# Kernel tuning notes

Measured on AMD Instinct MI355X. Metric: run time of the kernel, lower is better.

## Reference

```python
import jax, jax.numpy as jnp
import numpy as np

DT = 0.01
NUM_STEPS = 2
DIM = 8        # latentDim (q:4, p:4)
HID = 128      # hiddenDim
BATCH = 524288


def _hamiltonian(z, W1, b1, W2, b2, W3, b3):
    # MLP H: (batch, 8) -> (batch,) scalar energy, tanh activations
    h = jnp.tanh(z @ W1 + b1)
    h = jnp.tanh(h @ W2 + b2)
    return (h @ W3 + b3)[..., 0]


def _grad_h(z, W1, b1, W2, b2, W3, b3):
    # dH/dz, batched; mirrors torch.autograd.grad(H.sum(), z)
    # torch detaches z before grad (create_graph keeps param graph)
    zc = jax.lax.stop_gradient(z)
    return jax.grad(lambda zz: _hamiltonian(zz, W1, b1, W2, b2, W3, b3).sum())(zc)


def setup_inputs() -> dict:
    key = jax.random.key(0)
    ks = jax.random.split(key, 7)
    z = jax.random.normal(ks[0], (BATCH, DIM), dtype=jnp.float32)
    W1 = jax.random.normal(ks[1], (DIM, HID), dtype=jnp.float32) / np.float32(np.sqrt(DIM))
    b1 = jnp.zeros((HID,), dtype=jnp.float32)
    W2 = jax.random.normal(ks[2], (HID, HID), dtype=jnp.float32) / np.float32(np.sqrt(HID))
    b2 = jnp.zeros((HID,), dtype=jnp.float32)
    W3 = jax.random.normal(ks[3], (HID, 1), dtype=jnp.float32) / np.float32(np.sqrt(HID))
    b3 = jnp.zeros((1,), dtype=jnp.float32)
    return {"z": z, "W1": W1, "b1": b1, "W2": W2, "b2": b2, "W3": W3, "b3": b3}


def reference(z, W1, b1, W2, b2, W3, b3):
    q, p = jnp.split(z, 2, axis=1)
    for _ in range(NUM_STEPS):
        g = _grad_h(jnp.concatenate([q, p], axis=1), W1, b1, W2, b2, W3, b3)
        dHdq, dHdp = jnp.split(g, 2, axis=1)
        p_half = p - 0.5 * DT * dHdq
        q_new = q + DT * dHdp
        g2 = _grad_h(jnp.concatenate([q_new, p_half], axis=1), W1, b1, W2, b2, W3, b3)
        dHdq_new = jnp.split(g2, 2, axis=1)[0]
        p = p_half - 0.5 * DT * dHdq_new
        q = q_new
    return jnp.concatenate([q, p], axis=1)
```

## Files before the change

kernel.cpp:

```cpp
#include <hip/hip_runtime.h>


typedef float f32x4 __attribute__((ext_vector_type(4)));
typedef int   i32x2 __attribute__((ext_vector_type(2)));
typedef int   i32x4 __attribute__((ext_vector_type(4)));
typedef int   i32x8 __attribute__((ext_vector_type(8)));

#define DT 0.01f
#define S1 64.0f
#define S2 16.0f
#define TWO_LOG2E 2.8853900817779268f
#define SCL1 0x7F7F7F7F

#define OFF_W1B 0
#define OFF_W2B 4096
#define OFF_W2T 20480
#define OFF_W1T 36864
#define WTOT    38912

__device__ __forceinline__ unsigned char to_fp8(float x) {
    return (unsigned char)(__builtin_amdgcn_cvt_pk_fp8_f32(x, x, 0, false) & 0xff);
}
__device__ __forceinline__ float fexp2(float x) {
#if __has_builtin(__builtin_amdgcn_exp2f)
    return __builtin_amdgcn_exp2f(x);
#else
    return exp2f(x);
#endif
}
__device__ __forceinline__ float frcp(float x) {
#if __has_builtin(__builtin_amdgcn_rcpf)
    return __builtin_amdgcn_rcpf(x);
#else
    return 1.0f / x;
#endif
}

__device__ __forceinline__ i32x2 tr8(unsigned char* p) {
#if __has_builtin(__builtin_amdgcn_ds_read_tr8_b64)
    return __builtin_amdgcn_ds_read_tr8_b64((__attribute__((address_space(3))) i32x2*)p);
#else
    i32x2 d;
    asm volatile("ds_read_b64_tr_b8 %0, %1\n\ts_waitcnt lgkmcnt(0)"
                 : "=v"(d)
                 : "v"((unsigned)(unsigned long long)(__attribute__((address_space(3))) void*)p)
                 : "memory");
    __builtin_amdgcn_sched_barrier(0);
    return d;
#endif
}

__device__ __forceinline__ i32x8 read_a(unsigned char* abase) {
    i32x2 a0 = tr8(abase);
    i32x2 a1 = tr8(abase + 512);
    i32x2 a2 = tr8(abase + 1024);
    i32x2 a3 = tr8(abase + 1536);
    return (i32x8){a0[0], a0[1], a1[0], a1[1], a2[0], a2[1], a3[0], a3[1]};
}

__device__ __forceinline__ f32x4 mm128(i32x8 a, i32x8 b, f32x4 c) {
#if __has_builtin(__builtin_amdgcn_mfma_scale_f32_16x16x128_f8f6f4)
    return __builtin_amdgcn_mfma_scale_f32_16x16x128_f8f6f4(a, b, c, 0, 0, 0, SCL1, 0, SCL1);
#else
    #pragma unroll
    for (int kt = 0; kt < 4; kt++) {
        long long aa = ((long long)(unsigned)a[2 * kt + 1] << 32) | (unsigned)a[2 * kt];
        long long bb = ((long long)(unsigned)b[2 * kt + 1] << 32) | (unsigned)b[2 * kt];
        c = __builtin_amdgcn_mfma_f32_16x16x32_fp8_fp8(aa, bb, c, 0, 0, 0);
    }
    return c;
#endif
}

__global__ __launch_bounds__(256) void hnn_prep_kernel(
    const float* __restrict__ W1, const float* __restrict__ W2,
    unsigned char* __restrict__ ws)
{
    const int t = threadIdx.x, b = blockIdx.x;
    if (b == 0) {
        for (int i = t; i < 1024; i += 256) ((int*)(ws + OFF_W1B))[i] = 0;
        for (int i = t; i < 512;  i += 256) ((int*)(ws + OFF_W1T))[i] = 0;
        __syncthreads();
        for (int i = t; i < 1024; i += 256) {
            int row = i >> 7, col = i & 127;
            float w = W1[i];
            ws[OFF_W1B + (col >> 4) * 512 + (col & 15) * 8 + row] = to_fp8(w * TWO_LOG2E);
            int c = col >> 5, h = c >> 1, s = (c & 1) * 8 + (col & 7);
            int qd = (col >> 3) & 3;
            ws[OFF_W1T + (h * 64 + qd * 16 + row) * 16 + s] = to_fp8(w);
        }
    } else {
        int idx = (b - 1) * 256 + t;
        int row = idx >> 7, col = idx & 127;
        float w = W2[idx];
        {
            int c = row >> 5, h = c >> 1, s = (c & 1) * 8 + (row & 7);
            int qd = (row >> 3) & 3;
            ws[OFF_W2B + (((col >> 4) * 2 + h) * 64 + qd * 16 + (col & 15)) * 16 + s] =
                to_fp8(w * TWO_LOG2E);
        }
        {
            int c = col >> 5, h = c >> 1, s = (c & 1) * 8 + (col & 7);
            int qd = (col >> 3) & 3;
            ws[OFF_W2T + (((row >> 4) * 2 + h) * 64 + qd * 16 + (row & 15)) * 16 + s] =
                to_fp8(w * 4.0f);
        }
    }
}

__global__ __launch_bounds__(256) void hnn_leapfrog_kernel(
    const float* __restrict__ Z, const unsigned char* __restrict__ WS,
    const float* __restrict__ B1f, const float* __restrict__ B2f,
    const float* __restrict__ W3, float* __restrict__ OUT)
{
    __shared__ __align__(16) unsigned char sWT[WTOT];
    __shared__ __align__(16) unsigned char sACT[4 * 2048];
    __shared__ __align__(16) float sZ[512];

    const int t   = threadIdx.x;
    const int blk = blockIdx.x;

    for (int i = t; i < WTOT / 16; i += 256)
        __builtin_amdgcn_global_load_lds(
            (const __attribute__((address_space(1))) void*)(WS + i * 16),
            (__attribute__((address_space(3))) void*)(sWT + i * 16), 16, 0, 0);
    sZ[t]       = Z[blk * 512 + t];
    sZ[t + 256] = Z[blk * 512 + 256 + t];

    const int lane = t & 63;
    const int wv   = t >> 6;
    const int nn   = lane & 15;
    const int qd   = lane >> 4;

    float b1v[8], b2v[8], w3v[8];
    #pragma unroll
    for (int nt = 0; nt < 8; nt++) {
        b1v[nt] = B1f[nt * 16 + nn] * TWO_LOG2E;
        b2v[nt] = B2f[nt * 16 + nn] * TWO_LOG2E;
        w3v[nt] = W3[nt * 16 + nn] * (4.0f * S2);
    }
    __syncthreads();

    unsigned char* act   = sACT + wv * 2048;
    float*         zrow  = sZ + wv * 128;
    unsigned char* abase = act + qd * 128 + nn;
    unsigned char* awr   = act + nn * 16 + qd * 4;

    #pragma unroll 1
    for (int ev = 0; ev < 4; ev++) {
        long long az = 0;
        if (qd == 0) {
            const f32x4* zr = (const f32x4*)(zrow + nn * 8);
            f32x4 z0 = zr[0], z1 = zr[1];
            int lo = __builtin_amdgcn_cvt_pk_fp8_f32(z0[0], z0[1], 0, false);
            lo     = __builtin_amdgcn_cvt_pk_fp8_f32(z0[2], z0[3], lo, true);
            int hi = __builtin_amdgcn_cvt_pk_fp8_f32(z1[0], z1[1], 0, false);
            hi     = __builtin_amdgcn_cvt_pk_fp8_f32(z1[2], z1[3], hi, true);
            az = ((long long)(unsigned)hi << 32) | (unsigned)lo;
        }
        float hc[8][4];
        #pragma unroll
        for (int nt = 0; nt < 8; nt++) {
            long long bf = *(const long long*)(sWT + OFF_W1B + nt * 512 + lane * 8);
            f32x4 c = {b1v[nt], b1v[nt], b1v[nt], b1v[nt]};
            c = __builtin_amdgcn_mfma_f32_16x16x32_fp8_fp8(az, bf, c, 0, 0, 0);
            #pragma unroll
            for (int r = 0; r < 4; r++) {
                float e  = fexp2(c[r]);
                float rr = frcp(e + 1.0f);
                hc[nt][r] = fmaf(-2.0f, rr, 1.0f);
            }
            int v = __builtin_amdgcn_cvt_pk_fp8_f32(hc[nt][0], hc[nt][1], 0, false);
            v     = __builtin_amdgcn_cvt_pk_fp8_f32(hc[nt][2], hc[nt][3], v, true);
            *(int*)(awr + nt * 256) = v;
        }
        i32x8 a8 = read_a(abase);
        #pragma unroll
        for (int nt = 0; nt < 8; nt++) {
            i32x4 bA = *(const i32x4*)(sWT + OFF_W2B + nt * 2048 + lane * 16);
            i32x4 bB = *(const i32x4*)(sWT + OFF_W2B + nt * 2048 + 1024 + lane * 16);
            i32x8 b8 = {bA[0], bA[1], bA[2], bA[3], bB[0], bB[1], bB[2], bB[3]};
            f32x4 c = {b2v[nt], b2v[nt], b2v[nt], b2v[nt]};
            c = mm128(a8, b8, c);
            float dd[4];
            #pragma unroll
            for (int r = 0; r < 4; r++) {
                float e  = fexp2(c[r]);
                float rr = frcp(e + 1.0f);
                dd[r] = w3v[nt] * fmaf(-rr, rr, rr);
            }
            int v = __builtin_amdgcn_cvt_pk_fp8_f32(dd[0], dd[1], 0, false);
            v     = __builtin_amdgcn_cvt_pk_fp8_f32(dd[2], dd[3], v, true);
            *(int*)(awr + nt * 256) = v;
        }
        a8 = read_a(abase);
        #pragma unroll
        for (int nt = 0; nt < 8; nt++) {
            i32x4 bA = *(const i32x4*)(sWT + OFF_W2T + nt * 2048 + lane * 16);
            i32x4 bB = *(const i32x4*)(sWT + OFF_W2T + nt * 2048 + 1024 + lane * 16);
            i32x8 b8 = {bA[0], bA[1], bA[2], bA[3], bB[0], bB[1], bB[2], bB[3]};
            f32x4 c = {0.f, 0.f, 0.f, 0.f};
            c = mm128(a8, b8, c);
            float dd[4];
            #pragma unroll
            for (int r = 0; r < 4; r++) {
                float h = hc[nt][r];
                dd[r] = c[r] * fmaf(-h, h, 1.0f);
            }
            int v = __builtin_amdgcn_cvt_pk_fp8_f32(dd[0], dd[1], 0, false);
            v     = __builtin_amdgcn_cvt_pk_fp8_f32(dd[2], dd[3], v, true);
            *(int*)(awr + nt * 256) = v;
        }
        a8 = read_a(abase);
        i32x4 bA = *(const i32x4*)(sWT + OFF_W1T + lane * 16);
        i32x4 bB = *(const i32x4*)(sWT + OFF_W1T + 1024 + lane * 16);
        i32x8 b8 = {bA[0], bA[1], bA[2], bA[3], bB[0], bB[1], bB[2], bB[3]};
        f32x4 g = {0.f, 0.f, 0.f, 0.f};
        g = mm128(a8, b8, g);
        const bool first = (ev & 1) == 0;
        if (nn < 4) {
            float* p = zrow + qd * 32 + nn + 4;
            #pragma unroll
            for (int r = 0; r < 4; r++) p[r * 8] -= (0.5f * DT / S1) * g[r];
        } else if (nn < 8 && first) {
            float* p = zrow + qd * 32 + (nn - 4);
            #pragma unroll
            for (int r = 0; r < 4; r++) p[r * 8] += (DT / S1) * g[r];
        }
    }

    OUT[blk * 512 + wv * 128 + lane]      = zrow[lane];
    OUT[blk * 512 + wv * 128 + 64 + lane] = zrow[64 + lane];
}

extern "C" void kernel_launch(void* const* d_in, const int* in_sizes, int n_in,
                              void* d_out, int out_size, void* d_ws, size_t ws_size,
                              hipStream_t stream) {
    const float* Z  = (const float*)d_in[0];
    const float* W1 = (const float*)d_in[1];
    const float* B1 = (const float*)d_in[2];
    const float* W2 = (const float*)d_in[3];
    const float* B2 = (const float*)d_in[4];
    const float* W3 = (const float*)d_in[5];
    float* OUT = (float*)d_out;
    unsigned char* ws = (unsigned char*)d_ws;
    int blocks = in_sizes[0] / 512;
    hipLaunchKernelGGL(hnn_prep_kernel, dim3(65), dim3(256), 0, stream, W1, W2, ws);
    hipLaunchKernelGGL(hnn_leapfrog_kernel, dim3(blocks), dim3(256), 0, stream,
                       Z, ws, B1, B2, W3, OUT);
}
```

Measured before the change: 264.6 us.

## Fold W3 into W2T weights, factor bias exp, and double block size

W3 is folded into the transposed W2 fp8 weights during prep, which removes a per-element multiply in the layer-2 backward path. Bias addition is rewritten as a multiply by a precomputed exp2(bias), so MFMAs start from zero accumulators. Blocks now hold 512 threads (8 waves) to amortize the per-block LDS weight load over more rows. The W3 fold shifts fp8 scaling (256*W3 now sits inside fp8 weights), which can change precision, and the larger LDS footprint per block may lower occupancy.

```diff
diff --git a/kernel.cpp b/kernel.cpp
--- a/kernel.cpp
+++ b/kernel.cpp
@@ -8,7 +8,6 @@
 
 #define DT 0.01f
 #define S1 64.0f
-#define S2 16.0f
 #define TWO_LOG2E 2.8853900817779268f
 #define SCL1 0x7F7F7F7F
 
@@ -50,12 +49,18 @@
 #endif
 }
 
+__device__ __forceinline__ i32x8 cat44(i32x4 a, i32x4 b) {
+    return __builtin_shufflevector(a, b, 0, 1, 2, 3, 4, 5, 6, 7);
+}
+
 __device__ __forceinline__ i32x8 read_a(unsigned char* abase) {
     i32x2 a0 = tr8(abase);
     i32x2 a1 = tr8(abase + 512);
     i32x2 a2 = tr8(abase + 1024);
     i32x2 a3 = tr8(abase + 1536);
-    return (i32x8){a0[0], a0[1], a1[0], a1[1], a2[0], a2[1], a3[0], a3[1]};
+    i32x4 lo = __builtin_shufflevector(a0, a1, 0, 1, 2, 3);
+    i32x4 hi = __builtin_shufflevector(a2, a3, 0, 1, 2, 3);
+    return cat44(lo, hi);
 }
 
 __device__ __forceinline__ f32x4 mm128(i32x8 a, i32x8 b, f32x4 c) {
@@ -74,7 +79,7 @@
 
 __global__ __launch_bounds__(256) void hnn_prep_kernel(
     const float* __restrict__ W1, const float* __restrict__ W2,
-    unsigned char* __restrict__ ws)
+    const float* __restrict__ W3, unsigned char* __restrict__ ws)
 {
     const int t = threadIdx.x, b = blockIdx.x;
     if (b == 0) {
@@ -103,41 +108,40 @@
             int c = col >> 5, h = c >> 1, s = (c & 1) * 8 + (col & 7);
             int qd = (col >> 3) & 3;
             ws[OFF_W2T + (((row >> 4) * 2 + h) * 64 + qd * 16 + (row & 15)) * 16 + s] =
-                to_fp8(w * 4.0f);
-        }
-    }
-}
-
-__global__ __launch_bounds__(256) void hnn_leapfrog_kernel(
+                to_fp8(w * 256.0f * W3[col]);
+        }
+    }
+}
+
+__global__ __launch_bounds__(512) void hnn_leapfrog_kernel(
     const float* __restrict__ Z, const unsigned char* __restrict__ WS,
     const float* __restrict__ B1f, const float* __restrict__ B2f,
-    const float* __restrict__ W3, float* __restrict__ OUT)
+    float* __restrict__ OUT)
 {
     __shared__ __align__(16) unsigned char sWT[WTOT];
-    __shared__ __align__(16) unsigned char sACT[4 * 2048];
-    __shared__ __align__(16) float sZ[512];
+    __shared__ __align__(16) unsigned char sACT[8 * 2048];
+    __shared__ __align__(16) float sZ[1024];
 
     const int t   = threadIdx.x;
     const int blk = blockIdx.x;
 
-    for (int i = t; i < WTOT / 16; i += 256)
+    for (int i = t; i < WTOT / 16; i += 512)
         __builtin_amdgcn_global_load_lds(
             (const __attribute__((address_space(1))) void*)(WS + i * 16),
             (__attribute__((address_space(3))) void*)(sWT + i * 16), 16, 0, 0);
-    sZ[t]       = Z[blk * 512 + t];
-    sZ[t + 256] = Z[blk * 512 + 256 + t];
+    sZ[t]       = Z[blk * 1024 + t];
+    sZ[t + 512] = Z[blk * 1024 + 512 + t];
 
     const int lane = t & 63;
     const int wv   = t >> 6;
     const int nn   = lane & 15;
     const int qd   = lane >> 4;
 
-    float b1v[8], b2v[8], w3v[8];
+    float eb1v[8], eb2v[8];
     #pragma unroll
     for (int nt = 0; nt < 8; nt++) {
-        b1v[nt] = B1f[nt * 16 + nn] * TWO_LOG2E;
-        b2v[nt] = B2f[nt * 16 + nn] * TWO_LOG2E;
-        w3v[nt] = W3[nt * 16 + nn] * (4.0f * S2);
+        eb1v[nt] = fexp2(B1f[nt * 16 + nn] * TWO_LOG2E);
+        eb2v[nt] = fexp2(B2f[nt * 16 + nn] * TWO_LOG2E);
     }
     __syncthreads();
 
@@ -145,6 +149,10 @@
     float*         zrow  = sZ + wv * 128;
     unsigned char* abase = act + qd * 128 + nn;
     unsigned char* awr   = act + nn * 16 + qd * 4;
+    const unsigned char* w8  = sWT + lane * 8;
+    const unsigned char* w16 = sWT + lane * 16;
+
+    const f32x4 zc = {0.f, 0.f, 0.f, 0.f};
 
     #pragma unroll 1
     for (int ev = 0; ev < 4; ev++) {
@@ -161,13 +169,12 @@
         float hc[8][4];
         #pragma unroll
         for (int nt = 0; nt < 8; nt++) {
-            long long bf = *(const long long*)(sWT + OFF_W1B + nt * 512 + lane * 8);
-            f32x4 c = {b1v[nt], b1v[nt], b1v[nt], b1v[nt]};
-            c = __builtin_amdgcn_mfma_f32_16x16x32_fp8_fp8(az, bf, c, 0, 0, 0);
+            long long bf = *(const long long*)(w8 + OFF_W1B + nt * 512);
+            f32x4 c = __builtin_amdgcn_mfma_f32_16x16x32_fp8_fp8(az, bf, zc, 0, 0, 0);
             #pragma unroll
             for (int r = 0; r < 4; r++) {
                 float e  = fexp2(c[r]);
-                float rr = frcp(e + 1.0f);
+                float rr = frcp(fmaf(e, eb1v[nt], 1.0f));
                 hc[nt][r] = fmaf(-2.0f, rr, 1.0f);
             }
             int v = __builtin_amdgcn_cvt_pk_fp8_f32(hc[nt][0], hc[nt][1], 0, false);
@@ -177,17 +184,15 @@
         i32x8 a8 = read_a(abase);
         #pragma unroll
         for (int nt = 0; nt < 8; nt++) {
-            i32x4 bA = *(const i32x4*)(sWT + OFF_W2B + nt * 2048 + lane * 16);
-            i32x4 bB = *(const i32x4*)(sWT + OFF_W2B + nt * 2048 + 1024 + lane * 16);
-            i32x8 b8 = {bA[0], bA[1], bA[2], bA[3], bB[0], bB[1], bB[2], bB[3]};
-            f32x4 c = {b2v[nt], b2v[nt], b2v[nt], b2v[nt]};
-            c = mm128(a8, b8, c);
+            i32x4 bA = *(const i32x4*)(w16 + OFF_W2B + nt * 2048);
+            i32x4 bB = *(const i32x4*)(w16 + OFF_W2B + nt * 2048 + 1024);
+            f32x4 c = mm128(a8, cat44(bA, bB), zc);
             float dd[4];
             #pragma unroll
             for (int r = 0; r < 4; r++) {
                 float e  = fexp2(c[r]);
-                float rr = frcp(e + 1.0f);
-                dd[r] = w3v[nt] * fmaf(-rr, rr, rr);
+                float rr = frcp(fmaf(e, eb2v[nt], 1.0f));
+                dd[r] = fmaf(-rr, rr, rr);
             }
             int v = __builtin_amdgcn_cvt_pk_fp8_f32(dd[0], dd[1], 0, false);
             v     = __builtin_amdgcn_cvt_pk_fp8_f32(dd[2], dd[3], v, true);
@@ -196,11 +201,9 @@
         a8 = read_a(abase);
         #pragma unroll
         for (int nt = 0; nt < 8; nt++) {
-            i32x4 bA = *(const i32x4*)(sWT + OFF_W2T + nt * 2048 + lane * 16);
-            i32x4 bB = *(const i32x4*)(sWT + OFF_W2T + nt * 2048 + 1024 + lane * 16);
-            i32x8 b8 = {bA[0], bA[1], bA[2], bA[3], bB[0], bB[1], bB[2], bB[3]};
-            f32x4 c = {0.f, 0.f, 0.f, 0.f};
-            c = mm128(a8, b8, c);
+            i32x4 bA = *(const i32x4*)(w16 + OFF_W2T + nt * 2048);
+            i32x4 bB = *(const i32x4*)(w16 + OFF_W2T + nt * 2048 + 1024);
+            f32x4 c = mm128(a8, cat44(bA, bB), zc);
             float dd[4];
             #pragma unroll
             for (int r = 0; r < 4; r++) {
@@ -212,11 +215,9 @@
             *(int*)(awr + nt * 256) = v;
         }
         a8 = read_a(abase);
-        i32x4 bA = *(const i32x4*)(sWT + OFF_W1T + lane * 16);
-        i32x4 bB = *(const i32x4*)(sWT + OFF_W1T + 1024 + lane * 16);
-        i32x8 b8 = {bA[0], bA[1], bA[2], bA[3], bB[0], bB[1], bB[2], bB[3]};
-        f32x4 g = {0.f, 0.f, 0.f, 0.f};
-        g = mm128(a8, b8, g);
+        i32x4 bA = *(const i32x4*)(w16 + OFF_W1T);
+        i32x4 bB = *(const i32x4*)(w16 + OFF_W1T + 1024);
+        f32x4 g = mm128(a8, cat44(bA, bB), zc);
         const bool first = (ev & 1) == 0;
         if (nn < 4) {
             float* p = zrow + qd * 32 + nn + 4;
@@ -229,8 +230,8 @@
         }
     }
 
-    OUT[blk * 512 + wv * 128 + lane]      = zrow[lane];
-    OUT[blk * 512 + wv * 128 + 64 + lane] = zrow[64 + lane];
+    OUT[blk * 1024 + wv * 128 + lane]      = zrow[lane];
+    OUT[blk * 1024 + wv * 128 + 64 + lane] = zrow[64 + lane];
 }
 
 extern "C" void kernel_launch(void* const* d_in, const int* in_sizes, int n_in,
@@ -244,8 +245,8 @@
     const float* W3 = (const float*)d_in[5];
     float* OUT = (float*)d_out;
     unsigned char* ws = (unsigned char*)d_ws;
-    int blocks = in_sizes[0] / 512;
-    hipLaunchKernelGGL(hnn_prep_kernel, dim3(65), dim3(256), 0, stream, W1, W2, ws);
-    hipLaunchKernelGGL(hnn_leapfrog_kernel, dim3(blocks), dim3(256), 0, stream,
-                       Z, ws, B1, B2, W3, OUT);
-}
+    int blocks = in_sizes[0] / 1024;
+    hipLaunchKernelGGL(hnn_prep_kernel, dim3(65), dim3(256), 0, stream, W1, W2, W3, ws);
+    hipLaunchKernelGGL(hnn_leapfrog_kernel, dim3(blocks), dim3(512), 0, stream,
+                       Z, ws, B1, B2, OUT);
+}
```

New measurement: 240.2 us. 9.3% less time.
